# Kernel tuning notes

Hardware: AMD Instinct MI355X
Metric: run time of the kernel (lower is better)

## Reference

```python
import jax, jax.numpy as jnp
import numpy as np

N = 20000      # n_nodes
E = 320000     # n_edges (multiple of 4, so _from_coo drops nothing)
D = 512        # embed_dim
H = 8          # num_heads
DK = D // H    # d_k = 64


def setup_inputs() -> dict:
    key = jax.random.key(0)
    ks = jax.random.split(key, 12)
    x = jax.random.normal(ks[0], (N, D), jnp.float32)
    rows = jnp.sort(jax.random.randint(ks[1], (E,), 0, N))
    cols = jax.random.randint(ks[2], (E,), 0, N)
    edge_index = jnp.stack([rows, cols]).astype(jnp.int32)  # [2, E]
    att_bias = jax.random.normal(ks[3], (E, H), jnp.float32)
    s = float(1.0 / np.sqrt(D))  # ~xavier scale
    Wq = jax.random.normal(ks[4], (D, D), jnp.float32) * s
    Wk = jax.random.normal(ks[5], (D, D), jnp.float32) * s
    Wv = jax.random.normal(ks[6], (D, D), jnp.float32) * s
    Wo = jax.random.normal(ks[7], (D, D), jnp.float32) * s
    bq = jnp.zeros((D,), jnp.float32)
    bk = jnp.zeros((D,), jnp.float32)
    bv = jnp.zeros((D,), jnp.float32)
    bo = jnp.zeros((D,), jnp.float32)
    return dict(x=x, edge_index=edge_index, att_bias=att_bias,
                Wq=Wq, bq=bq, Wk=Wk, bk=bk, Wv=Wv, bv=bv, Wo=Wo, bo=bo)


def reference(x, edge_index, att_bias, Wq, bq, Wk, bk, Wv, bv, Wo, bo):
    n = x.shape[0]
    rows, cols = edge_index[0], edge_index[1]
    # per-head projections: [n, H, DK]
    q = (x @ Wq + bq).reshape(n, H, DK)
    k = (x @ Wk + bk).reshape(n, H, DK)
    v = (x @ Wv + bv).reshape(n, H, DK)
    scale = 1.0 / jnp.sqrt(jnp.asarray(DK, x.dtype))
    # masked QK^T on the edge pattern, plus additive bias: [E, H]
    logits = jnp.einsum('ehd,ehd->eh', q[rows] * scale, k[cols]) + att_bias
    # CSR (segment) softmax over each destination row
    row_max = jax.ops.segment_max(logits, rows, num_segments=n)      # [n, H]
    p = jnp.exp(logits - row_max[rows])                              # [E, H]
    denom = jax.ops.segment_sum(p, rows, num_segments=n)            # [n, H]
    att = p / denom[rows]                                            # [E, H]
    # sparse-dense bmm: y[i] = sum_{e: rows[e]=i} att[e] * v[cols[e]]
    y = jax.ops.segment_sum(att[:, :, None] * v[cols], rows, num_segments=n)  # [n, H, DK]
    out = y.reshape(n, H * DK) @ Wo + bo
    return out
```

## Files before the change

kernel.cpp:

```cpp
#include <hip/hip_runtime.h>
#include <hip/hip_bf16.h>

typedef unsigned short ushort_t;
typedef unsigned int uint32;
typedef __attribute__((ext_vector_type(8))) short short8;
typedef __attribute__((ext_vector_type(4))) float floatx4;

#define DEV __device__ __forceinline__

DEV float b2f(ushort_t u) { return __uint_as_float(((uint32)u) << 16); }
DEV ushort_t f2b(float f) {
  __hip_bfloat16 h = __float2bfloat16(f);
  return __builtin_bit_cast(unsigned short, h);
}
DEV void unpack8(const uint4& u, float* f) {
  f[0] = __uint_as_float(u.x << 16); f[1] = __uint_as_float(u.x & 0xffff0000u);
  f[2] = __uint_as_float(u.y << 16); f[3] = __uint_as_float(u.y & 0xffff0000u);
  f[4] = __uint_as_float(u.z << 16); f[5] = __uint_as_float(u.z & 0xffff0000u);
  f[6] = __uint_as_float(u.w << 16); f[7] = __uint_as_float(u.w & 0xffff0000u);
}
DEV void unpack_i8x8(uint2 u, float* f) {
  f[0] = (float)((int)(u.x << 24) >> 24);
  f[1] = (float)((int)(u.x << 16) >> 24);
  f[2] = (float)((int)(u.x << 8) >> 24);
  f[3] = (float)((int)u.x >> 24);
  f[4] = (float)((int)(u.y << 24) >> 24);
  f[5] = (float)((int)(u.y << 16) >> 24);
  f[6] = (float)((int)(u.y << 8) >> 24);
  f[7] = (float)((int)u.y >> 24);
}

#define GLOAD_LDS(gp, lp) \
  __builtin_amdgcn_global_load_lds((const __attribute__((address_space(1))) uint32*)(gp), \
                                   (__attribute__((address_space(3))) uint32*)(lp), 16, 0, 0)

#define KVROW 1088

__global__ __launch_bounds__(256) void k_detect(const ushort_t* __restrict__ x,
                                                int* __restrict__ flag) {
  __shared__ int red[256];
  int tid = threadIdx.x;
  int wild = 0;
  for (int i = tid; i < 4096; i += 256) {
    uint32 e = (x[i] >> 7) & 0xFFu;
    if (e < 100u || e > 140u) wild++;
  }
  red[tid] = wild;
  __syncthreads();
  for (int s = 128; s > 0; s >>= 1) {
    if (tid < s) red[tid] += red[tid + s];
    __syncthreads();
  }
  if (tid == 0) flag[0] = (red[0] > 400) ? 1 : 0;
}

__global__ __launch_bounds__(256) void k_transpose(
    const void* __restrict__ Wq, const void* __restrict__ Wk,
    const void* __restrict__ Wv, const void* __restrict__ Wo,
    ushort_t* __restrict__ WT4, const int* __restrict__ flagp) {
  __shared__ ushort_t t[32][33];
  int isf32 = *flagp;
  int z = blockIdx.z;
  const void* src = (z == 0) ? Wq : (z == 1) ? Wk : (z == 2) ? Wv : Wo;
  ushort_t* dst = WT4 + (size_t)z * 512 * 512;
  int bx = blockIdx.x, by = blockIdx.y;
  int tx = threadIdx.x, ty = threadIdx.y;
#pragma unroll
  for (int i = 0; i < 4; i++) {
    size_t idx = (size_t)(by * 32 + ty + 8 * i) * 512 + bx * 32 + tx;
    ushort_t v = isf32 ? f2b(((const float*)src)[idx]) : ((const ushort_t*)src)[idx];
    t[ty + 8 * i][tx] = v;
  }
  __syncthreads();
#pragma unroll
  for (int i = 0; i < 4; i++)
    dst[(size_t)(bx * 32 + ty + 8 * i) * 512 + by * 32 + tx] = t[tx][ty + 8 * i];
}

__global__ __launch_bounds__(256) void k_biases(
    const void* __restrict__ bq, const void* __restrict__ bk,
    const void* __restrict__ bv, const void* __restrict__ bo,
    float* __restrict__ biasf, const int* __restrict__ flagp) {
  int i = blockIdx.x * 256 + threadIdx.x;
  if (i >= 2048) return;
  int z = i >> 9, j = i & 511;
  const void* b = (z == 0) ? bq : (z == 1) ? bk : (z == 2) ? bv : bo;
  biasf[i] = (*flagp) ? ((const float*)b)[j] : b2f(((const ushort_t*)b)[j]);
}

__global__ __launch_bounds__(256) void k_convx(
    const void* __restrict__ x, ushort_t* __restrict__ xb, int n8,
    const int* __restrict__ flagp) {
  int i = blockIdx.x * 256 + threadIdx.x;
  if (i >= n8) return;
  if (*flagp) {
    const float* xf = (const float*)x + (size_t)i * 8;
    float4 f0 = ((const float4*)xf)[0];
    float4 f1 = ((const float4*)xf)[1];
    uint4 o;
    o.x = (uint32)f2b(f0.x) | ((uint32)f2b(f0.y) << 16);
    o.y = (uint32)f2b(f0.z) | ((uint32)f2b(f0.w) << 16);
    o.z = (uint32)f2b(f1.x) | ((uint32)f2b(f1.y) << 16);
    o.w = (uint32)f2b(f1.z) | ((uint32)f2b(f1.w) << 16);
    ((uint4*)xb)[i] = o;
  } else {
    ((uint4*)xb)[i] = ((const uint4*)x)[i];
  }
}

__global__ void k_build_rp(const int* __restrict__ rows, int E, int N, int* __restrict__ rp) {
  int i = blockIdx.x * blockDim.x + threadIdx.x;
  if (i > N) return;
  int lo = 0, hi = E;
  while (lo < hi) {
    int mid = (lo + hi) >> 1;
    if (rows[mid] < i) lo = mid + 1; else hi = mid;
  }
  rp[i] = lo;
}

DEV void gemm_body(const ushort_t* __restrict__ A, const ushort_t* __restrict__ BT,
                   const float* __restrict__ bias, void* C,
                   int M, int ldc, float scale, int row0, int by, int mode) {
  __shared__ ushort_t As[128 * 32];
  __shared__ ushort_t Bs[128 * 32];
  int tid = threadIdx.x;
  int w = tid >> 6, lane = tid & 63;
  int sr = lane >> 2;
  int sk = (lane & 3) * 8;

  floatx4 acc[4][4];
#pragma unroll
  for (int i = 0; i < 4; i++)
#pragma unroll
    for (int j = 0; j < 4; j++)
#pragma unroll
      for (int r = 0; r < 4; r++) acc[i][j][r] = 0.f;

  int lm = lane & 15, quad = lane >> 4;
  int wr = w >> 1, wc = w & 1;
  const int nG = by * 128 + w * 32;

  int rA0 = row0 + w * 32 + sr; if (rA0 >= M) rA0 = M - 1;
  int rA1 = rA0 + 16;          if (rA1 >= M) rA1 = M - 1;
  const ushort_t* gA0 = A + (size_t)rA0 * 512 + sk;
  const ushort_t* gA1 = A + (size_t)rA1 * 512 + sk;
  const ushort_t* gB0 = BT + (size_t)(nG + sr) * 512 + sk;
  const ushort_t* gB1 = BT + (size_t)(nG + 16 + sr) * 512 + sk;

  for (int k0 = 0; k0 < 512; k0 += 32) {
    GLOAD_LDS(gA0 + k0, As + (w * 32 + 0) * 32);
    GLOAD_LDS(gA1 + k0, As + (w * 32 + 16) * 32);
    GLOAD_LDS(gB0 + k0, Bs + (w * 32 + 0) * 32);
    GLOAD_LDS(gB1 + k0, Bs + (w * 32 + 16) * 32);
    __syncthreads();

    const ushort_t* pa = As + (wr * 64 + lm) * 32 + quad * 8;
    const ushort_t* pb = Bs + (wc * 64 + lm) * 32 + quad * 8;
    short8 af[4], bfr[4];
#pragma unroll
    for (int t4 = 0; t4 < 4; t4++) {
      af[t4]  = *(const short8*)(pa + t4 * 16 * 32);
      bfr[t4] = *(const short8*)(pb + t4 * 16 * 32);
    }
#pragma unroll
    for (int mt = 0; mt < 4; mt++)
#pragma unroll
      for (int nt = 0; nt < 4; nt++)
        acc[mt][nt] = __builtin_amdgcn_mfma_f32_16x16x32_bf16(af[mt], bfr[nt], acc[mt][nt], 0, 0, 0);
    __syncthreads();
  }

  int colB = by * 128 + wc * 64 + lm;
  float bv4[4];
#pragma unroll
  for (int nt = 0; nt < 4; nt++) bv4[nt] = bias[colB + nt * 16];

  if (mode <= 1) {
#pragma unroll
    for (int mt = 0; mt < 4; mt++) {
      int rg0 = row0 + wr * 64 + mt * 16 + quad * 4;
#pragma unroll
      for (int nt = 0; nt < 4; nt++) {
#pragma unroll
        for (int r = 0; r < 4; r++) {
          int rg = rg0 + r;
          if (rg < M) {
            float val = (acc[mt][nt][r] + bv4[nt]) * scale;
            size_t off = (size_t)rg * ldc + colB + nt * 16;
            if (mode == 1) ((float*)C)[off] = val;
            else           ((ushort_t*)C)[off] = f2b(val);
          }
        }
      }
    }
  } else {
    int vslot = (mode == 4);
    int colbase = by * 128 + wc * 64;
    int head = colbase >> 6;
#pragma unroll
    for (int mt = 0; mt < 4; mt++) {
#pragma unroll
      for (int r = 0; r < 4; r++) {
        int rg = row0 + wr * 64 + mt * 16 + quad * 4 + r;
        float v0 = acc[mt][0][r] + bv4[0];
        float v1 = acc[mt][1][r] + bv4[1];
        float v2 = acc[mt][2][r] + bv4[2];
        float v3 = acc[mt][3][r] + bv4[3];
        float am = fmaxf(fmaxf(fabsf(v0), fabsf(v1)), fmaxf(fabsf(v2), fabsf(v3)));
        am = fmaxf(am, __shfl_xor(am, 1));
        am = fmaxf(am, __shfl_xor(am, 2));
        am = fmaxf(am, __shfl_xor(am, 4));
        am = fmaxf(am, __shfl_xor(am, 8));
        am = fmaxf(am, 1e-20f);
        float inv8 = 127.0f / am;
        float sc8 = am * (1.0f / 127.0f);
        if (rg < M) {
          unsigned char* Crow = (unsigned char*)C + (size_t)rg * KVROW + colbase + (vslot ? 512 : 0);
          Crow[lm +  0] = (unsigned char)(signed char)(int)rintf(v0 * inv8);
          Crow[lm + 16] = (unsigned char)(signed char)(int)rintf(v1 * inv8);
          Crow[lm + 32] = (unsigned char)(signed char)(int)rintf(v2 * inv8);
          Crow[lm + 48] = (unsigned char)(signed char)(int)rintf(v3 * inv8);
          if (lm == 0)
            *(float*)((unsigned char*)C + (size_t)rg * KVROW + 1024 + head * 8 + vslot * 4) = sc8;
        }
      }
    }
  }
}

__global__ __launch_bounds__(256) void k_gemm_qkv(
    const ushort_t* __restrict__ xb, const ushort_t* __restrict__ WT4,
    const float* __restrict__ biasf, ushort_t* Qp, unsigned char* KV8, int M) {
  int z = blockIdx.z;
  const ushort_t* BT = WT4 + (size_t)z * 512 * 512;
  const float* bias = biasf + (size_t)z * 512;
  if (z == 0)
    gemm_body(xb, BT, bias, Qp, M, 512, 0.125f, blockIdx.x * 128, blockIdx.y, 0);
  else
    gemm_body(xb, BT, bias, KV8, M, 0, 1.0f, blockIdx.x * 128, blockIdx.y, z == 1 ? 3 : 4);
}

__global__ __launch_bounds__(256) void k_gemm_out(
    const ushort_t* __restrict__ y, const ushort_t* __restrict__ WT4,
    const float* __restrict__ biasf, void* out, int M,
    const int* __restrict__ flagp) {
  gemm_body(y, WT4 + (size_t)3 * 512 * 512, biasf + 3 * 512, out, M, 512, 1.0f,
            blockIdx.x * 128, blockIdx.y, *flagp);
}

__global__ __launch_bounds__(256) void k_edge(
    ushort_t* Qy, const unsigned char* __restrict__ KV8,
    const void* __restrict__ ab, const int* __restrict__ cols,
    const int* __restrict__ rp, int Nn, int E, const int* __restrict__ flagp) {
  int node = blockIdx.x * 4 + (threadIdx.x >> 6);
  if (node >= Nn) return;
  int lane = threadIdx.x & 63;
  int h8 = lane >> 3;
  int isf32 = *flagp;

  uint4 qu = ((const uint4*)(Qy + (size_t)node * 512))[lane];
  float qf[8];
  unpack8(qu, qf);

  int e0 = rp[node], e1 = rp[node + 1];
  int cnt = e1 - e0;

  float s0 = 0.f, s1 = 0.f;
  float acc0[8], acc1[8];
#pragma unroll
  for (int j = 0; j < 8; j++) { acc0[j] = 0.f; acc1[j] = 0.f; }

  uint2 kb[4], vb[4];
  float2 scb[4];
  float abf[4];

  auto pref = [&](int t, int slot) {
    int valid = t < cnt;
    int ei = valid ? (e0 + t) : e0;
    int c = valid ? cols[ei] : 0;
    const unsigned char* kvrow = KV8 + (size_t)c * KVROW;
    kb[slot] = *(const uint2*)(kvrow + lane * 8);
    vb[slot] = *(const uint2*)(kvrow + 512 + lane * 8);
    scb[slot] = *(const float2*)(kvrow + 1024 + h8 * 8);
    size_t bi = (size_t)ei * 8 + h8;
    float a = isf32 ? ((const float*)ab)[bi] : b2f(((const ushort_t*)ab)[bi]);
    abf[slot] = valid ? a : -1e30f;
  };
  auto consume = [&](int slot, float* acc, float& s) {
    float kf[8];
    unpack_i8x8(kb[slot], kf);
    float d = 0.f;
#pragma unroll
    for (int j = 0; j < 8; j++) d = fmaf(qf[j], kf[j], d);
    d += __shfl_xor(d, 1);
    d += __shfl_xor(d, 2);
    d += __shfl_xor(d, 4);
    float logit = fminf(fmaf(d, scb[slot].x, abf[slot]), 80.f);
    float pw = __expf(logit);
    s += pw;
    float pwv = pw * scb[slot].y;
    float vf[8];
    unpack_i8x8(vb[slot], vf);
#pragma unroll
    for (int j = 0; j < 8; j++) acc[j] = fmaf(pwv, vf[j], acc[j]);
  };

  pref(0, 0); pref(1, 1); pref(2, 2); pref(3, 3);
  int iters = (cnt + 3) >> 2;
  for (int it = 0; it < iters; ++it) {
    int nt = it * 4 + 4;
    consume(0, acc0, s0); pref(nt + 0, 0);
    consume(1, acc1, s1); pref(nt + 1, 1);
    consume(2, acc0, s0); pref(nt + 2, 2);
    consume(3, acc1, s1); pref(nt + 3, 3);
  }

  float s = s0 + s1;
  float inv = (cnt > 0 && s > 0.f) ? 1.f / s : 0.f;
  ushort_t hb[8];
#pragma unroll
  for (int j = 0; j < 8; j++) hb[j] = f2b((acc0[j] + acc1[j]) * inv);
  uint4 uh;
  uh.x = (uint32)hb[0] | ((uint32)hb[1] << 16);
  uh.y = (uint32)hb[2] | ((uint32)hb[3] << 16);
  uh.z = (uint32)hb[4] | ((uint32)hb[5] << 16);
  uh.w = (uint32)hb[6] | ((uint32)hb[7] << 16);
  ((uint4*)(Qy + (size_t)node * 512))[lane] = uh;
}

extern "C" void kernel_launch(void* const* d_in, const int* in_sizes, int n_in,
                              void* d_out, int out_size, void* d_ws, size_t ws_size,
                              hipStream_t stream) {
  const void* x  = d_in[0];
  const int* ei  = (const int*)d_in[1];
  const void* ab = d_in[2];
  const void* Wq = d_in[3];
  const void* bq = d_in[4];
  const void* Wk = d_in[5];
  const void* bk = d_in[6];
  const void* Wv = d_in[7];
  const void* bv = d_in[8];
  const void* Wo = d_in[9];
  const void* bo = d_in[10];

  const int D = 512;
  int M = in_sizes[0] / D;
  int E = in_sizes[1] / 2;
  const int* rows = ei;
  const int* cols = ei + E;

  char* p = (char*)d_ws;
  size_t off = 0;
  auto carve = [&](size_t bytes) -> void* {
    off = (off + 255) & ~(size_t)255;
    void* r = p + off;
    off += bytes;
    return r;
  };
  int* flag          = (int*)carve(4);
  ushort_t* WT4      = (ushort_t*)carve((size_t)4 * 512 * 512 * 2);
  float* biasf       = (float*)carve((size_t)4 * 512 * 4);
  ushort_t* xb       = (ushort_t*)carve((size_t)M * 512 * 2);
  ushort_t* Qp       = (ushort_t*)carve((size_t)M * 512 * 2);
  unsigned char* KV8 = (unsigned char*)carve((size_t)M * KVROW);
  int* rp            = (int*)carve((size_t)(M + 1) * 4);
  (void)ws_size;

  k_detect<<<1, 256, 0, stream>>>((const ushort_t*)x, flag);
  k_transpose<<<dim3(16, 16, 4), dim3(32, 8), 0, stream>>>(Wq, Wk, Wv, Wo, WT4, flag);
  k_biases<<<8, 256, 0, stream>>>(bq, bk, bv, bo, biasf, flag);
  int n8 = M * 512 / 8;
  k_convx<<<(n8 + 255) / 256, 256, 0, stream>>>(x, xb, n8, flag);
  k_build_rp<<<(M + 1 + 255) / 256, 256, 0, stream>>>(rows, E, M, rp);

  int rb = (M + 127) / 128;
  k_gemm_qkv<<<dim3(rb, 4, 3), 256, 0, stream>>>(xb, WT4, biasf, Qp, KV8, M);
  k_edge<<<(M + 3) / 4, 256, 0, stream>>>(Qp, KV8, ab, cols, rp, M, E, flag);
  k_gemm_out<<<dim3(rb, 4, 1), 256, 0, stream>>>(Qp, WT4, biasf, d_out, M, flag);
}
```

Baseline: 298.6 us.

## Process four edges per wave in edge kernel with wider per-lane loads

The edge kernel now gives each 16-lane quarter of a wave its own edge, so a wave handles four edges at once. Each lane holds 32 q values and loads 32-byte K/V chunks as two uint4 reads, using a double-buffered prefetch. The per-head dot-product reduction drops to one shuffle, but partial sums must be reduced across quarters with extra shuffles at the end. The int8 KV row layout is reorganised so the scales come first and K/V follow at 64/576 offsets. The larger register footprint (32 accumulators plus 32 q values) may lower occupancy.

```diff
diff --git a/kernel.cpp b/kernel.cpp
--- a/kernel.cpp
+++ b/kernel.cpp
@@ -19,15 +19,11 @@
   f[4] = __uint_as_float(u.z << 16); f[5] = __uint_as_float(u.z & 0xffff0000u);
   f[6] = __uint_as_float(u.w << 16); f[7] = __uint_as_float(u.w & 0xffff0000u);
 }
-DEV void unpack_i8x8(uint2 u, float* f) {
-  f[0] = (float)((int)(u.x << 24) >> 24);
-  f[1] = (float)((int)(u.x << 16) >> 24);
-  f[2] = (float)((int)(u.x << 8) >> 24);
-  f[3] = (float)((int)u.x >> 24);
-  f[4] = (float)((int)(u.y << 24) >> 24);
-  f[5] = (float)((int)(u.y << 16) >> 24);
-  f[6] = (float)((int)(u.y << 8) >> 24);
-  f[7] = (float)((int)u.y >> 24);
+DEV void unpack_i8x4(uint32 u, float* f) {
+  f[0] = (float)((int)(u << 24) >> 24);
+  f[1] = (float)((int)(u << 16) >> 24);
+  f[2] = (float)((int)(u << 8) >> 24);
+  f[3] = (float)((int)u >> 24);
 }
 
 #define GLOAD_LDS(gp, lp) \
@@ -35,6 +31,8 @@
                                    (__attribute__((address_space(3))) uint32*)(lp), 16, 0, 0)
 
 #define KVROW 1088
+#define KOFF 64
+#define VOFF 576
 
 __global__ __launch_bounds__(256) void k_detect(const ushort_t* __restrict__ x,
                                                 int* __restrict__ flag) {
@@ -216,13 +214,14 @@
         float inv8 = 127.0f / am;
         float sc8 = am * (1.0f / 127.0f);
         if (rg < M) {
-          unsigned char* Crow = (unsigned char*)C + (size_t)rg * KVROW + colbase + (vslot ? 512 : 0);
+          unsigned char* base = (unsigned char*)C + (size_t)rg * KVROW;
+          unsigned char* Crow = base + (vslot ? VOFF : KOFF) + colbase;
           Crow[lm +  0] = (unsigned char)(signed char)(int)rintf(v0 * inv8);
           Crow[lm + 16] = (unsigned char)(signed char)(int)rintf(v1 * inv8);
           Crow[lm + 32] = (unsigned char)(signed char)(int)rintf(v2 * inv8);
           Crow[lm + 48] = (unsigned char)(signed char)(int)rintf(v3 * inv8);
           if (lm == 0)
-            *(float*)((unsigned char*)C + (size_t)rg * KVROW + 1024 + head * 8 + vslot * 4) = sc8;
+            *(float*)(base + head * 8 + vslot * 4) = sc8;
         }
       }
     }
@@ -256,77 +255,116 @@
   int node = blockIdx.x * 4 + (threadIdx.x >> 6);
   if (node >= Nn) return;
   int lane = threadIdx.x & 63;
-  int h8 = lane >> 3;
+  int sl = lane & 15;
+  int q4 = lane >> 4;
+  int hq = sl >> 1;
   int isf32 = *flagp;
 
-  uint4 qu = ((const uint4*)(Qy + (size_t)node * 512))[lane];
-  float qf[8];
-  unpack8(qu, qf);
+  float qf[32];
+  {
+    const uint4* qp = (const uint4*)(Qy + (size_t)node * 512 + sl * 32);
+#pragma unroll
+    for (int i = 0; i < 4; i++) {
+      uint4 qu = qp[i];
+      unpack8(qu, qf + i * 8);
+    }
+  }
 
   int e0 = rp[node], e1 = rp[node + 1];
   int cnt = e1 - e0;
 
-  float s0 = 0.f, s1 = 0.f;
-  float acc0[8], acc1[8];
-#pragma unroll
-  for (int j = 0; j < 8; j++) { acc0[j] = 0.f; acc1[j] = 0.f; }
-
-  uint2 kb[4], vb[4];
-  float2 scb[4];
-  float abf[4];
-
-  auto pref = [&](int t, int slot) {
+  float s = 0.f;
+  float acc[32];
+#pragma unroll
+  for (int j = 0; j < 32; j++) acc[j] = 0.f;
+
+  uint4 kb[2][2], vb[2][2];
+  float ks[2], vs[2], abf[2];
+
+  auto pref = [&](int g, int st) {
+    int t = g * 4 + q4;
     int valid = t < cnt;
     int ei = valid ? (e0 + t) : e0;
     int c = valid ? cols[ei] : 0;
-    const unsigned char* kvrow = KV8 + (size_t)c * KVROW;
-    kb[slot] = *(const uint2*)(kvrow + lane * 8);
-    vb[slot] = *(const uint2*)(kvrow + 512 + lane * 8);
-    scb[slot] = *(const float2*)(kvrow + 1024 + h8 * 8);
-    size_t bi = (size_t)ei * 8 + h8;
+    const unsigned char* row = KV8 + (size_t)c * KVROW;
+    const uint4* kp = (const uint4*)(row + KOFF + sl * 32);
+    kb[st][0] = kp[0];
+    kb[st][1] = kp[1];
+    const uint4* vp = (const uint4*)(row + VOFF + sl * 32);
+    vb[st][0] = vp[0];
+    vb[st][1] = vp[1];
+    float2 sc = *(const float2*)(row + hq * 8);
+    ks[st] = sc.x;
+    vs[st] = sc.y;
+    size_t bi = (size_t)ei * 8 + hq;
     float a = isf32 ? ((const float*)ab)[bi] : b2f(((const ushort_t*)ab)[bi]);
-    abf[slot] = valid ? a : -1e30f;
+    abf[st] = valid ? a : -1e30f;
   };
-  auto consume = [&](int slot, float* acc, float& s) {
-    float kf[8];
-    unpack_i8x8(kb[slot], kf);
+
+  auto consume = [&](int st) {
     float d = 0.f;
-#pragma unroll
-    for (int j = 0; j < 8; j++) d = fmaf(qf[j], kf[j], d);
+    uint32 kw[8];
+    *(uint4*)(kw + 0) = kb[st][0];
+    *(uint4*)(kw + 4) = kb[st][1];
+#pragma unroll
+    for (int cch = 0; cch < 8; cch++) {
+      float kf[4];
+      unpack_i8x4(kw[cch], kf);
+#pragma unroll
+      for (int j = 0; j < 4; j++) d = fmaf(qf[cch * 4 + j], kf[j], d);
+    }
     d += __shfl_xor(d, 1);
-    d += __shfl_xor(d, 2);
-    d += __shfl_xor(d, 4);
-    float logit = fminf(fmaf(d, scb[slot].x, abf[slot]), 80.f);
+    float logit = fminf(fmaf(d, ks[st], abf[st]), 80.f);
     float pw = __expf(logit);
     s += pw;
-    float pwv = pw * scb[slot].y;
-    float vf[8];
-    unpack_i8x8(vb[slot], vf);
-#pragma unroll
-    for (int j = 0; j < 8; j++) acc[j] = fmaf(pwv, vf[j], acc[j]);
+    float pwv = pw * vs[st];
+    uint32 vw[8];
+    *(uint4*)(vw + 0) = vb[st][0];
+    *(uint4*)(vw + 4) = vb[st][1];
+#pragma unroll
+    for (int cch = 0; cch < 8; cch++) {
+      float vf[4];
+      unpack_i8x4(vw[cch], vf);
+#pragma unroll
+      for (int j = 0; j < 4; j++) acc[cch * 4 + j] = fmaf(pwv, vf[j], acc[cch * 4 + j]);
+    }
   };
 
-  pref(0, 0); pref(1, 1); pref(2, 2); pref(3, 3);
-  int iters = (cnt + 3) >> 2;
-  for (int it = 0; it < iters; ++it) {
-    int nt = it * 4 + 4;
-    consume(0, acc0, s0); pref(nt + 0, 0);
-    consume(1, acc1, s1); pref(nt + 1, 1);
-    consume(2, acc0, s0); pref(nt + 2, 2);
-    consume(3, acc1, s1); pref(nt + 3, 3);
-  }
-
-  float s = s0 + s1;
+  int groups = (cnt + 3) >> 2;
+  if (groups > 0) {
+    pref(0, 0);
+    for (int g = 0; g < groups; ++g) {
+      int st = g & 1;
+      if (g + 1 < groups) pref(g + 1, st ^ 1);
+      consume(st);
+    }
+  }
+
+  s += __shfl_xor(s, 16);
+  s += __shfl_xor(s, 32);
+#pragma unroll
+  for (int j = 0; j < 32; j++) {
+    acc[j] += __shfl_xor(acc[j], 16);
+    acc[j] += __shfl_xor(acc[j], 32);
+  }
+
   float inv = (cnt > 0 && s > 0.f) ? 1.f / s : 0.f;
-  ushort_t hb[8];
-#pragma unroll
-  for (int j = 0; j < 8; j++) hb[j] = f2b((acc0[j] + acc1[j]) * inv);
-  uint4 uh;
-  uh.x = (uint32)hb[0] | ((uint32)hb[1] << 16);
-  uh.y = (uint32)hb[2] | ((uint32)hb[3] << 16);
-  uh.z = (uint32)hb[4] | ((uint32)hb[5] << 16);
-  uh.w = (uint32)hb[6] | ((uint32)hb[7] << 16);
-  ((uint4*)(Qy + (size_t)node * 512))[lane] = uh;
+  if (q4 == 0) {
+    uint4 o[4];
+#pragma unroll
+    for (int i = 0; i < 4; i++) {
+      ushort_t hb[8];
+#pragma unroll
+      for (int j = 0; j < 8; j++) hb[j] = f2b(acc[i * 8 + j] * inv);
+      o[i].x = (uint32)hb[0] | ((uint32)hb[1] << 16);
+      o[i].y = (uint32)hb[2] | ((uint32)hb[3] << 16);
+      o[i].z = (uint32)hb[4] | ((uint32)hb[5] << 16);
+      o[i].w = (uint32)hb[6] | ((uint32)hb[7] << 16);
+    }
+    uint4* yp = (uint4*)(Qy + (size_t)node * 512 + sl * 32);
+#pragma unroll
+    for (int i = 0; i < 4; i++) yp[i] = o[i];
+  }
 }
 
 extern "C" void kernel_launch(void* const* d_in, const int* in_sizes, int n_in,
```

New measurement: 325.0 us. 8.8% more time.
